# Performance work log

Measured on AMD Instinct MI355X. Metric: run time of the kernel, lower is better.

The kernel has to match this reference:

```python
import jax, jax.numpy as jnp
import numpy as np

B, R, S = 4, 32768, 64
NEAR, FAR = -1.5, 1.5
DELTA_INF = 1e10
EPS = 1e-10


def setup_inputs() -> dict:
    key = jax.random.key(0)
    k1, k2 = jax.random.split(key)
    rgb = jax.random.uniform(k1, (B, R, S, 3), dtype=jnp.float32)
    sigma = jax.random.normal(k2, (B, R, S, 1), dtype=jnp.float32)
    # stratified-like depths: monotonically increasing along sample axis per ray
    z_steps = jnp.linspace(0.0, 1.0, S, dtype=jnp.float32)  # [S]
    z_vals = (NEAR * (1.0 - z_steps) + FAR * z_steps)[None, None, :, None]
    z_vals = jnp.broadcast_to(z_vals, (B, R, S, 1)).astype(jnp.float32)
    return {"rgb": rgb, "sigma": sigma, "z_vals": z_vals}


def reference(rgb, sigma, z_vals):
    """fancy_integration with clamp_mode='relu', noise_std=0, white_back=False, last_back=False.

    rgb:    [B, R, S, 3]
    sigma:  [B, R, S, 1]
    z_vals: [B, R, S, 1] (sorted along S)
    Returns (rgb_final [B,R,3], depth_final [B,R,1], weights [B,R,S,1]).
    """
    # deltas between consecutive samples; last delta is 'infinite'
    deltas = z_vals[:, :, 1:] - z_vals[:, :, :-1]                      # [B,R,S-1,1]
    delta_inf = jnp.full_like(deltas[:, :, :1], DELTA_INF)
    deltas = jnp.concatenate([deltas, delta_inf], axis=2)              # [B,R,S,1]

    # sigma -> alpha: 1 - exp(-relu(sigma) * delta)
    alphas = 1.0 - jnp.exp(-deltas * jax.nn.relu(sigma))               # [B,R,S,1]

    # exclusive cumprod transmittance along sample axis
    alphas_shifted = jnp.concatenate(
        [jnp.ones_like(alphas[:, :, :1]), 1.0 - alphas + EPS], axis=2)  # [B,R,S+1,1]
    transmittance = jnp.cumprod(alphas_shifted, axis=2)[:, :, :-1]      # [B,R,S,1]
    weights = alphas * transmittance                                    # [B,R,S,1]

    rgb_final = jnp.sum(weights * rgb, axis=2)      # [B,R,3]
    depth_final = jnp.sum(weights * z_vals, axis=2)  # [B,R,1]
    return (rgb_final, depth_final, weights)
```

## Files before the change

kernel.cpp:

```cpp
#include <hip/hip_runtime.h>


#define NSAMP 64
#define EPS_W 1e-10f
#define DELTA_INF_V 1e10f

#define DPP_ROW_SHR(n)  (0x110 | (n))
#define DPP_ROW_BCAST15 0x142
#define DPP_ROW_BCAST31 0x143
#define DPP_WAVE_SHL1   0x130
#define DPP_WAVE_SHR1   0x138

template <int CTRL, int RM, int BM>
__device__ __forceinline__ float dpp_mov(float x, float old) {
    return __builtin_bit_cast(float,
        __builtin_amdgcn_update_dpp(
            __builtin_bit_cast(int, old), __builtin_bit_cast(int, x),
            CTRL, RM, BM, false));
}

__device__ __forceinline__ float scan_mul64(float p) {
    p *= dpp_mov<DPP_ROW_SHR(1), 0xf, 0xf>(p, 1.0f);
    p *= dpp_mov<DPP_ROW_SHR(2), 0xf, 0xf>(p, 1.0f);
    p *= dpp_mov<DPP_ROW_SHR(4), 0xf, 0xf>(p, 1.0f);
    p *= dpp_mov<DPP_ROW_SHR(8), 0xf, 0xf>(p, 1.0f);
    p *= dpp_mov<DPP_ROW_BCAST15, 0xa, 0xf>(p, 1.0f);
    p *= dpp_mov<DPP_ROW_BCAST31, 0xc, 0xf>(p, 1.0f);
    return p;
}

__device__ __forceinline__ float scan_add64(float x) {
    x += dpp_mov<DPP_ROW_SHR(1), 0xf, 0xf>(x, 0.0f);
    x += dpp_mov<DPP_ROW_SHR(2), 0xf, 0xf>(x, 0.0f);
    x += dpp_mov<DPP_ROW_SHR(4), 0xf, 0xf>(x, 0.0f);
    x += dpp_mov<DPP_ROW_SHR(8), 0xf, 0xf>(x, 0.0f);
    x += dpp_mov<DPP_ROW_BCAST15, 0xa, 0xf>(x, 0.0f);
    x += dpp_mov<DPP_ROW_BCAST31, 0xc, 0xf>(x, 0.0f);
    return x;
}

__global__ __launch_bounds__(256) void volrend_kernel(
    const float* __restrict__ rgb,
    const float* __restrict__ sigma,
    const float* __restrict__ z_vals,
    float* __restrict__ rgb_out,
    float* __restrict__ depth_out,
    float* __restrict__ weights_out,
    int n_rays)
{
    const int lane = threadIdx.x & 63;
    const int wave = threadIdx.x >> 6;
    const int ray  = blockIdx.x * (blockDim.x >> 6) + wave;
    if (ray >= n_rays) return;

    const long long base = (long long)ray * NSAMP + lane;

    const float sg = sigma[base];
    const float z  = z_vals[base];
    const float* rp = rgb + base * 3;
    const float cr = rp[0];
    const float cg = rp[1];
    const float cb = rp[2];

    const float z_next = dpp_mov<DPP_WAVE_SHL1, 0xf, 0xf>(z, 0.0f);
    const float delta  = (lane == NSAMP - 1) ? DELTA_INF_V : (z_next - z);

    const float alpha = 1.0f - __expf(-delta * fmaxf(sg, 0.0f));

    const float p = scan_mul64(1.0f - alpha + EPS_W);
    const float T = dpp_mov<DPP_WAVE_SHR1, 0xf, 0xf>(p, 1.0f);

    const float w = alpha * T;

    weights_out[base] = w;

    const float sr = scan_add64(w * cr);
    const float sg2 = scan_add64(w * cg);
    const float sb = scan_add64(w * cb);
    const float sd = scan_add64(w * z);

    if (lane == NSAMP - 1) {
        rgb_out[(long long)ray * 3 + 0] = sr;
        rgb_out[(long long)ray * 3 + 1] = sg2;
        rgb_out[(long long)ray * 3 + 2] = sb;
        depth_out[ray] = sd;
    }
}

extern "C" void kernel_launch(void* const* d_in, const int* in_sizes, int n_in,
                              void* d_out, int out_size, void* d_ws, size_t ws_size,
                              hipStream_t stream) {
    const float* rgb    = (const float*)d_in[0];
    const float* sigma  = (const float*)d_in[1];
    const float* z_vals = (const float*)d_in[2];

    const int n_rays = in_sizes[1] / NSAMP;

    float* out         = (float*)d_out;
    float* rgb_out     = out;
    float* depth_out   = out + (long long)n_rays * 3;
    float* weights_out = out + (long long)n_rays * 4;

    const int block = 256;
    const int rays_per_block = block / 64;
    const int grid = (n_rays + rays_per_block - 1) / rays_per_block;

    volrend_kernel<<<grid, block, 0, stream>>>(
        rgb, sigma, z_vals, rgb_out, depth_out, weights_out, n_rays);
}
```

Before: 199.6 us.

## Process multiple rays per wave with software-prefetched next-ray loads

Each wave now handles 16 consecutive rays in a loop instead of one, and loads the next ray's sigma, z and rgb before computing the current ray. The aim is to amortize launch and wave setup and to overlap global memory latency with the DPP scan work. The trade-off is a grid 16x smaller, so fewer waves are resident to hide latency, plus a redundant load on the final iteration.

```diff
diff --git a/kernel.cpp b/kernel.cpp
--- a/kernel.cpp
+++ b/kernel.cpp
@@ -4,6 +4,7 @@
 #define NSAMP 64
 #define EPS_W 1e-10f
 #define DELTA_INF_V 1e10f
+#define IT 16
 
 #define DPP_ROW_SHR(n)  (0x110 | (n))
 #define DPP_ROW_BCAST15 0x142
@@ -50,40 +51,55 @@
 {
     const int lane = threadIdx.x & 63;
     const int wave = threadIdx.x >> 6;
-    const int ray  = blockIdx.x * (blockDim.x >> 6) + wave;
+    const int waves_per_block = blockDim.x >> 6;
+    const long long wave_g = (long long)blockIdx.x * waves_per_block + wave;
+
+    long long ray = wave_g * IT;
     if (ray >= n_rays) return;
+    const long long ray_end = (ray + IT < n_rays) ? ray + IT : n_rays;
 
-    const long long base = (long long)ray * NSAMP + lane;
+    {
+        const long long base = ray * NSAMP + lane;
+        const float* rp = rgb + base * 3;
+        float sg = sigma[base];
+        float z  = z_vals[base];
+        float cr = rp[0], cg = rp[1], cb = rp[2];
 
-    const float sg = sigma[base];
-    const float z  = z_vals[base];
-    const float* rp = rgb + base * 3;
-    const float cr = rp[0];
-    const float cg = rp[1];
-    const float cb = rp[2];
+        #pragma unroll 1
+        for (;;) {
+            const long long nray  = ray + 1;
+            const long long pbase = ((nray < ray_end) ? nray : ray) * NSAMP + lane;
+            const float* prp = rgb + pbase * 3;
+            const float n_sg = sigma[pbase];
+            const float n_z  = z_vals[pbase];
+            const float n_cr = prp[0], n_cg = prp[1], n_cb = prp[2];
 
-    const float z_next = dpp_mov<DPP_WAVE_SHL1, 0xf, 0xf>(z, 0.0f);
-    const float delta  = (lane == NSAMP - 1) ? DELTA_INF_V : (z_next - z);
+            const float z_next = dpp_mov<DPP_WAVE_SHL1, 0xf, 0xf>(z, 0.0f);
+            const float delta  = (lane == NSAMP - 1) ? DELTA_INF_V : (z_next - z);
+            const float alpha  = 1.0f - __expf(-delta * fmaxf(sg, 0.0f));
 
-    const float alpha = 1.0f - __expf(-delta * fmaxf(sg, 0.0f));
+            const float p = scan_mul64(1.0f - alpha + EPS_W);
+            const float T = dpp_mov<DPP_WAVE_SHR1, 0xf, 0xf>(p, 1.0f);
+            const float w = alpha * T;
 
-    const float p = scan_mul64(1.0f - alpha + EPS_W);
-    const float T = dpp_mov<DPP_WAVE_SHR1, 0xf, 0xf>(p, 1.0f);
+            weights_out[ray * NSAMP + lane] = w;
 
-    const float w = alpha * T;
+            const float sr  = scan_add64(w * cr);
+            const float sg2 = scan_add64(w * cg);
+            const float sb  = scan_add64(w * cb);
+            const float sd  = scan_add64(w * z);
 
-    weights_out[base] = w;
+            if (lane == NSAMP - 1) {
+                rgb_out[ray * 3 + 0] = sr;
+                rgb_out[ray * 3 + 1] = sg2;
+                rgb_out[ray * 3 + 2] = sb;
+                depth_out[ray] = sd;
+            }
 
-    const float sr = scan_add64(w * cr);
-    const float sg2 = scan_add64(w * cg);
-    const float sb = scan_add64(w * cb);
-    const float sd = scan_add64(w * z);
-
-    if (lane == NSAMP - 1) {
-        rgb_out[(long long)ray * 3 + 0] = sr;
-        rgb_out[(long long)ray * 3 + 1] = sg2;
-        rgb_out[(long long)ray * 3 + 2] = sb;
-        depth_out[ray] = sd;
+            if (nray >= ray_end) break;
+            ray = nray;
+            sg = n_sg; z = n_z; cr = n_cr; cg = n_cg; cb = n_cb;
+        }
     }
 }
 
@@ -102,7 +118,7 @@
     float* weights_out = out + (long long)n_rays * 4;
 
     const int block = 256;
-    const int rays_per_block = block / 64;
+    const int rays_per_block = (block / 64) * IT;
     const int grid = (n_rays + rays_per_block - 1) / rays_per_block;
 
     volrend_kernel<<<grid, block, 0, stream>>>(
```

New measurement: 215.2 us. +7.8%, slower.

## Process four samples per lane with float4 loads and row-level DPP scans

Applied to the files above, without the earlier changes.

Each wave now handles four rays, one per 16-lane DPP row, and each lane holds four consecutive samples loaded with float4 vector loads, including a 12-float RGB chunk. The transmittance product is computed serially within a lane, then scanned across the row with four DPP steps, replacing the six-step wave-wide scans. The color and depth sums are reduced the same way. This cuts instruction count and memory transactions per sample and issues wider coalesced accesses, at the cost of more registers per lane and an assumption that 16-byte alignment and four-ray grouping divide the input evenly.

```diff
diff --git a/kernel.cpp b/kernel.cpp
--- a/kernel.cpp
+++ b/kernel.cpp
@@ -1,41 +1,33 @@
 #include <hip/hip_runtime.h>
 
 
-#define NSAMP 64
 #define EPS_W 1e-10f
 #define DELTA_INF_V 1e10f
 
-#define DPP_ROW_SHR(n)  (0x110 | (n))
-#define DPP_ROW_BCAST15 0x142
-#define DPP_ROW_BCAST31 0x143
-#define DPP_WAVE_SHL1   0x130
-#define DPP_WAVE_SHR1   0x138
+#define DPP_ROW_SHL(n) (0x100 | (n))
+#define DPP_ROW_SHR(n) (0x110 | (n))
 
-template <int CTRL, int RM, int BM>
+template <int CTRL>
 __device__ __forceinline__ float dpp_mov(float x, float old) {
     return __builtin_bit_cast(float,
         __builtin_amdgcn_update_dpp(
             __builtin_bit_cast(int, old), __builtin_bit_cast(int, x),
-            CTRL, RM, BM, false));
+            CTRL, 0xf, 0xf, false));
 }
 
-__device__ __forceinline__ float scan_mul64(float p) {
-    p *= dpp_mov<DPP_ROW_SHR(1), 0xf, 0xf>(p, 1.0f);
-    p *= dpp_mov<DPP_ROW_SHR(2), 0xf, 0xf>(p, 1.0f);
-    p *= dpp_mov<DPP_ROW_SHR(4), 0xf, 0xf>(p, 1.0f);
-    p *= dpp_mov<DPP_ROW_SHR(8), 0xf, 0xf>(p, 1.0f);
-    p *= dpp_mov<DPP_ROW_BCAST15, 0xa, 0xf>(p, 1.0f);
-    p *= dpp_mov<DPP_ROW_BCAST31, 0xc, 0xf>(p, 1.0f);
+__device__ __forceinline__ float row_scan_mul(float p) {
+    p *= dpp_mov<DPP_ROW_SHR(1)>(p, 1.0f);
+    p *= dpp_mov<DPP_ROW_SHR(2)>(p, 1.0f);
+    p *= dpp_mov<DPP_ROW_SHR(4)>(p, 1.0f);
+    p *= dpp_mov<DPP_ROW_SHR(8)>(p, 1.0f);
     return p;
 }
 
-__device__ __forceinline__ float scan_add64(float x) {
-    x += dpp_mov<DPP_ROW_SHR(1), 0xf, 0xf>(x, 0.0f);
-    x += dpp_mov<DPP_ROW_SHR(2), 0xf, 0xf>(x, 0.0f);
-    x += dpp_mov<DPP_ROW_SHR(4), 0xf, 0xf>(x, 0.0f);
-    x += dpp_mov<DPP_ROW_SHR(8), 0xf, 0xf>(x, 0.0f);
-    x += dpp_mov<DPP_ROW_BCAST15, 0xa, 0xf>(x, 0.0f);
-    x += dpp_mov<DPP_ROW_BCAST31, 0xc, 0xf>(x, 0.0f);
+__device__ __forceinline__ float row_sum(float x) {
+    x += dpp_mov<DPP_ROW_SHR(1)>(x, 0.0f);
+    x += dpp_mov<DPP_ROW_SHR(2)>(x, 0.0f);
+    x += dpp_mov<DPP_ROW_SHR(4)>(x, 0.0f);
+    x += dpp_mov<DPP_ROW_SHR(8)>(x, 0.0f);
     return x;
 }
 
@@ -50,40 +42,71 @@
 {
     const int lane = threadIdx.x & 63;
     const int wave = threadIdx.x >> 6;
-    const int ray  = blockIdx.x * (blockDim.x >> 6) + wave;
+    const long long wave_g = (long long)blockIdx.x * (blockDim.x >> 6) + wave;
+
+    const int j   = lane & 15;
+    const int row = lane >> 4;
+    const long long ray = wave_g * 4 + row;
     if (ray >= n_rays) return;
 
-    const long long base = (long long)ray * NSAMP + lane;
+    const float4 sg = *(reinterpret_cast<const float4*>(sigma  + wave_g * 256) + lane);
+    const float4 zz = *(reinterpret_cast<const float4*>(z_vals + wave_g * 256) + lane);
+    const float4* rgb4 = reinterpret_cast<const float4*>(rgb + wave_g * 768 + (long long)lane * 12);
+    const float4 c0 = rgb4[0];
+    const float4 c1 = rgb4[1];
+    const float4 c2 = rgb4[2];
 
-    const float sg = sigma[base];
-    const float z  = z_vals[base];
-    const float* rp = rgb + base * 3;
-    const float cr = rp[0];
-    const float cg = rp[1];
-    const float cb = rp[2];
+    const float zn = dpp_mov<DPP_ROW_SHL(1)>(zz.x, 0.0f);
+    const float d0 = zz.y - zz.x;
+    const float d1 = zz.z - zz.y;
+    const float d2 = zz.w - zz.z;
+    const float d3 = (j == 15) ? DELTA_INF_V : (zn - zz.w);
 
-    const float z_next = dpp_mov<DPP_WAVE_SHL1, 0xf, 0xf>(z, 0.0f);
-    const float delta  = (lane == NSAMP - 1) ? DELTA_INF_V : (z_next - z);
+    const float a0 = 1.0f - __expf(-d0 * fmaxf(sg.x, 0.0f));
+    const float a1 = 1.0f - __expf(-d1 * fmaxf(sg.y, 0.0f));
+    const float a2 = 1.0f - __expf(-d2 * fmaxf(sg.z, 0.0f));
+    const float a3 = 1.0f - __expf(-d3 * fmaxf(sg.w, 0.0f));
 
-    const float alpha = 1.0f - __expf(-delta * fmaxf(sg, 0.0f));
+    const float q0 = 1.0f - a0 + EPS_W;
+    const float q1 = 1.0f - a1 + EPS_W;
+    const float q2 = 1.0f - a2 + EPS_W;
+    const float q3 = 1.0f - a3 + EPS_W;
+    const float P0 = q0;
+    const float P1 = P0 * q1;
+    const float P2 = P1 * q2;
+    const float P3 = P2 * q3;
 
-    const float p = scan_mul64(1.0f - alpha + EPS_W);
-    const float T = dpp_mov<DPP_WAVE_SHR1, 0xf, 0xf>(p, 1.0f);
+    const float R = row_scan_mul(P3);
+    const float E = dpp_mov<DPP_ROW_SHR(1)>(R, 1.0f);
 
-    const float w = alpha * T;
+    const float T0 = E;
+    const float T1 = E * P0;
+    const float T2 = E * P1;
+    const float T3 = E * P2;
 
-    weights_out[base] = w;
+    const float w0 = a0 * T0;
+    const float w1 = a1 * T1;
+    const float w2 = a2 * T2;
+    const float w3 = a3 * T3;
 
-    const float sr = scan_add64(w * cr);
-    const float sg2 = scan_add64(w * cg);
-    const float sb = scan_add64(w * cb);
-    const float sd = scan_add64(w * z);
+    float4 wv; wv.x = w0; wv.y = w1; wv.z = w2; wv.w = w3;
+    *(reinterpret_cast<float4*>(weights_out + wave_g * 256) + lane) = wv;
 
-    if (lane == NSAMP - 1) {
-        rgb_out[(long long)ray * 3 + 0] = sr;
-        rgb_out[(long long)ray * 3 + 1] = sg2;
-        rgb_out[(long long)ray * 3 + 2] = sb;
-        depth_out[ray] = sd;
+    float pr = w0 * c0.x + w1 * c0.w + w2 * c1.z + w3 * c2.y;
+    float pg = w0 * c0.y + w1 * c1.x + w2 * c1.w + w3 * c2.z;
+    float pb = w0 * c0.z + w1 * c1.y + w2 * c2.x + w3 * c2.w;
+    float pd = w0 * zz.x + w1 * zz.y + w2 * zz.z + w3 * zz.w;
+
+    pr = row_sum(pr);
+    pg = row_sum(pg);
+    pb = row_sum(pb);
+    pd = row_sum(pd);
+
+    if (j == 15) {
+        rgb_out[ray * 3 + 0] = pr;
+        rgb_out[ray * 3 + 1] = pg;
+        rgb_out[ray * 3 + 2] = pb;
+        depth_out[ray] = pd;
     }
 }
 
@@ -94,7 +117,7 @@
     const float* sigma  = (const float*)d_in[1];
     const float* z_vals = (const float*)d_in[2];
 
-    const int n_rays = in_sizes[1] / NSAMP;
+    const int n_rays = in_sizes[1] / 64;
 
     float* out         = (float*)d_out;
     float* rgb_out     = out;
@@ -102,7 +125,7 @@
     float* weights_out = out + (long long)n_rays * 4;
 
     const int block = 256;
-    const int rays_per_block = block / 64;
+    const int rays_per_block = (block / 64) * 4;
     const int grid = (n_rays + rays_per_block - 1) / rays_per_block;
 
     volrend_kernel<<<grid, block, 0, stream>>>(
```

After: 200.5 us. No clear change (+0.5%).
